# Kernel tuning notes

Measured on AMD Instinct MI355X. Metric: run time of the kernel, lower is better.

## Reference

```python
import jax, jax.numpy as jnp
import numpy as np
from jax import lax

ORDER = 2  # diffusion order per support, as in __init__(order=2)


def setup_inputs() -> dict:
    key = jax.random.key(0)
    k1, k2, k3 = jax.random.split(key, 3)
    N, C, V, L = 64, 32, 512, 13
    S, Kt, C_out = 3, 3, 32
    C_cat = (ORDER * S + 1) * C  # 224
    x = jax.random.normal(k1, (N, C, V, L), dtype=jnp.float32)
    support = jax.random.uniform(k2, (S, V, V), dtype=jnp.float32)
    # Conv2d(c_in=224, c_out=32, kernel=(1,Kt)) weights, PyTorch OIHW layout
    W = jax.random.normal(k3, (C_out, C_cat, 1, Kt), dtype=jnp.float32) * 0.02
    b = jnp.zeros((C_out,), dtype=jnp.float32)
    return {"x": x, "support": support, "W": W, "b": b}


def _nconv(x, A):
    # torch: A = A.T; einsum('ncvl,vw->ncwl', x, A.T)
    # => out[n,c,w,l] = sum_v A[w,v] * x[n,c,v,l]
    return jnp.einsum('ncvl,wv->ncwl', x, A)


def reference(x, support, W, b):
    out = [x]
    for s in range(support.shape[0]):  # small fixed support_len=3
        A = support[s]
        x1 = _nconv(x, A)
        out.append(x1)
        for _ in range(2, ORDER + 1):
            x1 = _nconv(x1, A)
            out.append(x1)
    h = jnp.concatenate(out, axis=1)  # [N, (order*S+1)*C, V, L]
    # Conv2d kernel (1, Kt), no padding, stride 1 -> temporal conv
    y = lax.conv_general_dilated(
        h, W, window_strides=(1, 1), padding='VALID',
        dimension_numbers=('NCHW', 'OIHW', 'NCHW'))
    y = y + b[None, :, None, None]
    # dropout is identity in eval mode
    return y
```

## Files before the change

kernel.cpp:

```cpp
#include <hip/hip_runtime.h>

typedef __attribute__((ext_vector_type(4))) float f32x4;
typedef __attribute__((ext_vector_type(8))) __bf16 bf16x8;
typedef __attribute__((ext_vector_type(4))) __bf16 bf16x4;
typedef __attribute__((ext_vector_type(4))) int i32x4;

#define SXE (26624 * 512)
#define AMS 262144

__global__ __launch_bounds__(256)
void prep_x(const float* __restrict__ x, __bf16* __restrict__ Xv2,
            const float* __restrict__ A, __bf16* __restrict__ Ab) {
  const int vt = blockIdx.x, n = blockIdx.y, tid = threadIdx.x;
  if (vt < 12) {
    const int i = (n * 12 + vt) * 256 + tid;
    const float4 f = ((const float4*)A)[i];
    bf16x4 o;
    o[0] = (__bf16)f.x; o[1] = (__bf16)f.y; o[2] = (__bf16)f.z; o[3] = (__bf16)f.w;
    ((bf16x4*)Ab)[i] = o;
  }
  __shared__ float Xs[32 * 209];
  const float* src = x + ((size_t)n * 32) * 6656 + vt * 16 * 13;
  for (int i = tid; i < 32 * 208; i += 256) {
    const int c = i / 208, r = i - c * 208;
    Xs[c * 209 + r] = src[(size_t)c * 6656 + r];
  }
  __syncthreads();
  for (int j = tid; j < 416; j += 256) {
    const int c = j & 31, l = j >> 5;
    bf16x8 o8[2];
    #pragma unroll
    for (int v = 0; v < 16; ++v) o8[v >> 3][v & 7] = (__bf16)Xs[c * 209 + v * 13 + l];
    __bf16* d = Xv2 + (((size_t)n * 13 + l) * 32 + c) * 512 + vt * 16;
    *(bf16x8*)d = o8[0];
    *(bf16x8*)(d + 8) = o8[1];
  }
}

__global__ __launch_bounds__(256)
void transA(const float* __restrict__ A, __bf16* __restrict__ Abt) {
  const int ut = blockIdx.x, vt = blockIdx.y, s = blockIdx.z, tid = threadIdx.x;
  __shared__ float T[64][65];
  const float* Asrc = A + (size_t)s * AMS;
  #pragma unroll
  for (int p = 0; p < 16; ++p) {
    const int rv = p * 4 + (tid >> 6), cu = tid & 63;
    T[rv][cu] = Asrc[(size_t)(vt * 64 + rv) * 512 + ut * 64 + cu];
  }
  __syncthreads();
  #pragma unroll
  for (int p = 0; p < 16; ++p) {
    const int ru = p * 4 + (tid >> 6), cv = tid & 63;
    Abt[(size_t)s * AMS + (size_t)(ut * 64 + ru) * 512 + vt * 64 + cv] = (__bf16)T[cv][ru];
  }
}

__global__ __launch_bounds__(512, 2)
void gemm_asq(const __bf16* __restrict__ Abt, const __bf16* __restrict__ Ab,
              __bf16* __restrict__ Ab2) {
  extern __shared__ char gsm[];
  const int tid = threadIdx.x;
  const int lane = tid & 63, wid = tid >> 6, q = lane >> 4, r16 = lane & 15;
  const int bx = blockIdx.x, by = blockIdx.y, s = blockIdx.z;

  const __bf16* Amat = Abt + (size_t)s * AMS;
  const __bf16* B = Ab + (size_t)s * AMS;
  __bf16* D = Ab2 + (size_t)s * AMS;

  const int W0 = by * 256, B0 = bx * 256;
  const int wm = wid >> 2, wn = wid & 3;
  const int srow = lane >> 3, spos = lane & 7;

  f32x4 acc[8][4];
  #pragma unroll
  for (int m = 0; m < 8; ++m)
    #pragma unroll
    for (int n = 0; n < 4; ++n) acc[m][n] = {0.f, 0.f, 0.f, 0.f};

  auto STAGE = [&](int bufsel, int kt) {
    const int k0 = kt * 64;
    char* As = gsm + bufsel * 65536;
    char* Bs = As + 32768;
    #pragma unroll
    for (int i = 0; i < 4; ++i) {
      const int slot = i * 8 + wid;
      const int r = slot * 8 + srow;
      const int gc = spos ^ (r & 7);
      const __bf16* ga = Amat + (size_t)(W0 + r) * 512 + k0 + gc * 8;
      const __bf16* gb = B    + (size_t)(B0 + r) * 512 + k0 + gc * 8;
      __builtin_amdgcn_global_load_lds((const __attribute__((address_space(1))) unsigned int*)ga,
                                       (__attribute__((address_space(3))) unsigned int*)(As + slot * 1024 + lane * 16),
                                       16, 0, 0);
      __builtin_amdgcn_global_load_lds((const __attribute__((address_space(1))) unsigned int*)gb,
                                       (__attribute__((address_space(3))) unsigned int*)(Bs + slot * 1024 + lane * 16),
                                       16, 0, 0);
    }
  };

  STAGE(0, 0);
  __syncthreads();
  for (int t = 0; t < 8; ++t) {
    const int cur = t & 1;
    if (t < 7) STAGE(cur ^ 1, t + 1);
    const char* As = gsm + cur * 65536;
    const char* Bs = As + 32768;
    #pragma unroll
    for (int ks = 0; ks < 2; ++ks) {
      const int ch = ks * 4 + q;
      bf16x8 af[4], df[8];
      #pragma unroll
      for (int n = 0; n < 4; ++n) {
        const int r = wn * 64 + n * 16 + r16;
        af[n] = *(const bf16x8*)(As + r * 128 + ((ch ^ (r & 7)) << 4));
      }
      #pragma unroll
      for (int m = 0; m < 8; ++m) {
        const int r = wm * 128 + m * 16 + r16;
        df[m] = *(const bf16x8*)(Bs + r * 128 + ((ch ^ (r & 7)) << 4));
      }
      #pragma unroll
      for (int m = 0; m < 8; ++m)
        #pragma unroll
        for (int n = 0; n < 4; ++n)
          acc[m][n] = __builtin_amdgcn_mfma_f32_16x16x32_bf16(af[n], df[m], acc[m][n], 0, 0, 0);
    }
    __syncthreads();
  }
  #pragma unroll
  for (int m = 0; m < 8; ++m) {
    const int b = B0 + wm * 128 + m * 16 + r16;
    #pragma unroll
    for (int n = 0; n < 4; ++n) {
      const int w = W0 + wn * 64 + n * 16 + q * 4;
      bf16x4 o4;
      o4[0] = (__bf16)acc[m][n][0]; o4[1] = (__bf16)acc[m][n][1];
      o4[2] = (__bf16)acc[m][n][2]; o4[3] = (__bf16)acc[m][n][3];
      *(bf16x4*)(D + (size_t)b * 512 + w) = o4;
    }
  }
}

__global__ __launch_bounds__(512, 2)
void gemm_bf16(const __bf16* __restrict__ Ab, const __bf16* __restrict__ Ab2,
               const __bf16* __restrict__ SRC, __bf16* __restrict__ Yb, int cpx) {
  extern __shared__ char gsm[];
  const int tid = threadIdx.x;
  const int lane = tid & 63, wid = tid >> 6, q = lane >> 4, r16 = lane & 15;

  const int bid = blockIdx.x;
  const int lg = (bid & 7) * cpx + (bid >> 3);
  const int bx = lg / 12, r12 = lg % 12, z = r12 >> 1, by = r12 & 1;

  const __bf16* Amat = (z < 3) ? (Ab + (size_t)z * AMS) : (Ab2 + (size_t)(z - 3) * AMS);
  const __bf16* B = SRC;
  __bf16* D = Yb + (size_t)z * SXE;

  const int W0 = by * 256, B0 = bx * 256;
  const int wm = wid >> 2, wn = wid & 3;
  const int srow = lane >> 3, spos = lane & 7;

  f32x4 acc[8][4];
  #pragma unroll
  for (int m = 0; m < 8; ++m)
    #pragma unroll
    for (int n = 0; n < 4; ++n) acc[m][n] = {0.f, 0.f, 0.f, 0.f};

  auto STAGE = [&](int bufsel, int kt) {
    const int k0 = kt * 64;
    char* As = gsm + bufsel * 65536;
    char* Bs = As + 32768;
    #pragma unroll
    for (int i = 0; i < 4; ++i) {
      const int slot = i * 8 + wid;
      const int r = slot * 8 + srow;
      const int gc = spos ^ (r & 7);
      const __bf16* ga = Amat + (size_t)(W0 + r) * 512 + k0 + gc * 8;
      const __bf16* gb = B    + (size_t)(B0 + r) * 512 + k0 + gc * 8;
      __builtin_amdgcn_global_load_lds((const __attribute__((address_space(1))) unsigned int*)ga,
                                       (__attribute__((address_space(3))) unsigned int*)(As + slot * 1024 + lane * 16),
                                       16, 0, 0);
      __builtin_amdgcn_global_load_lds((const __attribute__((address_space(1))) unsigned int*)gb,
                                       (__attribute__((address_space(3))) unsigned int*)(Bs + slot * 1024 + lane * 16),
                                       16, 0, 0);
    }
  };

  STAGE(0, 0);
  __syncthreads();

  for (int t = 0; t < 8; ++t) {
    const int cur = t & 1;
    if (t < 7) STAGE(cur ^ 1, t + 1);
    const char* As = gsm + cur * 65536;
    const char* Bs = As + 32768;
    #pragma unroll
    for (int ks = 0; ks < 2; ++ks) {
      const int ch = ks * 4 + q;
      bf16x8 af[4], df[8];
      #pragma unroll
      for (int n = 0; n < 4; ++n) {
        const int r = wn * 64 + n * 16 + r16;
        af[n] = *(const bf16x8*)(As + r * 128 + ((ch ^ (r & 7)) << 4));
      }
      #pragma unroll
      for (int m = 0; m < 8; ++m) {
        const int r = wm * 128 + m * 16 + r16;
        df[m] = *(const bf16x8*)(Bs + r * 128 + ((ch ^ (r & 7)) << 4));
      }
      __builtin_amdgcn_s_setprio(1);
      #pragma unroll
      for (int m = 0; m < 8; ++m)
        #pragma unroll
        for (int n = 0; n < 4; ++n)
          acc[m][n] = __builtin_amdgcn_mfma_f32_16x16x32_bf16(af[n], df[m], acc[m][n], 0, 0, 0);
      __builtin_amdgcn_s_setprio(0);
    }
    __syncthreads();
  }

  #pragma unroll
  for (int m = 0; m < 8; ++m) {
    const int b = B0 + wm * 128 + m * 16 + r16;
    #pragma unroll
    for (int n = 0; n < 4; ++n) {
      const int w = W0 + wn * 64 + n * 16 + q * 4;
      bf16x4 o4;
      o4[0] = (__bf16)acc[m][n][0]; o4[1] = (__bf16)acc[m][n][1];
      o4[2] = (__bf16)acc[m][n][2]; o4[3] = (__bf16)acc[m][n][3];
      *(bf16x4*)(D + (size_t)b * 512 + w) = o4;
    }
  }
}

__global__ __launch_bounds__(256, 2)
void conv_kernel(const __bf16* __restrict__ Xv2, const __bf16* __restrict__ Y1,
                 const __bf16* __restrict__ Y2, const float* __restrict__ W,
                 const float* __restrict__ bias, float* __restrict__ y) {
  const int vt = blockIdx.x;
  const int n  = blockIdx.y;
  const int tid = threadIdx.x;
  const int lane = tid & 63, wave = tid >> 6, q = lane >> 4, r16 = lane & 15;

  __shared__ char sm[59392];
  char* Ws = sm + 53248;

  const __bf16* gsrc[7] = {Xv2, Y1, Y2, Y1 + (size_t)SXE, Y2 + (size_t)SXE,
                           Y1 + 2 * (size_t)SXE, Y2 + 2 * (size_t)SXE};

  f32x4 acc[11][2];
  #pragma unroll
  for (int t = 0; t < 11; ++t) { acc[t][0] = {0,0,0,0}; acc[t][1] = {0,0,0,0}; }

  const int vv = wave * 16 + r16;
  const int vch = vv >> 3;
  const int vlo = (vv & 7) * 2;
  const int cst = tid >> 3, hst = tid & 7;
  const size_t goff = ((size_t)cst << 9) + hst * 8;
  const int lds_off = cst * 128 + ((hst ^ ((cst >> 3) << 1)) << 4);
  const int gbase = q * 1024 + (((vch ^ (q << 1)) & 7) << 4) + vlo;

  const size_t base = ((size_t)n * 416) * 512 + vt * 64;

  i32x4 hreg[13];
  {
    const __bf16* src = gsrc[0] + base;
    #pragma unroll
    for (int l = 0; l < 13; ++l)
      hreg[l] = *(const i32x4*)(src + (size_t)l * 16384 + goff);
  }

  for (int g = 0; g < 7; ++g) {
    __syncthreads();
    #pragma unroll
    for (int l = 0; l < 13; ++l)
      *(i32x4*)(sm + l * 4096 + lds_off) = hreg[l];
    for (int idx = tid; idx < 768; idx += 256) {
      const int f = idx >> 7, rem2 = idx & 127, lw = rem2 >> 1, half = rem2 & 1;
      const int kt = f >> 1, of = f & 1;
      const int o = of * 16 + (lw & 15);
      const int cc = g * 32 + (lw >> 4) * 8 + half * 4;
      bf16x4 w4;
      #pragma unroll
      for (int j = 0; j < 4; ++j)
        w4[j] = (__bf16)W[((size_t)o * 224 + cc + j) * 3 + kt];
      *(bf16x4*)(Ws + idx * 8) = w4;
    }
    __syncthreads();

    if (g < 6) {
      const __bf16* srcn = gsrc[g + 1] + base;
      #pragma unroll
      for (int l = 0; l < 13; ++l)
        hreg[l] = *(const i32x4*)(srcn + (size_t)l * 16384 + goff);
    }

    bf16x8 a8[13];
    #pragma unroll
    for (int l = 0; l < 13; ++l) {
      bf16x8 a;
      #pragma unroll
      for (int j = 0; j < 8; ++j)
        a[j] = *(const __bf16*)(sm + l * 4096 + gbase + j * 128);
      a8[l] = a;
    }
    bf16x8 wf[6];
    #pragma unroll
    for (int f = 0; f < 6; ++f)
      wf[f] = *(const bf16x8*)(Ws + (f * 64 + lane) * 16);

    #pragma unroll
    for (int kt = 0; kt < 3; ++kt)
      #pragma unroll
      for (int of = 0; of < 2; ++of)
        #pragma unroll
        for (int t = 0; t < 11; ++t)
          acc[t][of] = __builtin_amdgcn_mfma_f32_16x16x32_bf16(a8[t + kt], wf[kt * 2 + of], acc[t][of], 0, 0, 0);
  }

  float* Ds = (float*)sm;
  const int o16 = lane & 15;
  #pragma unroll
  for (int p = 0; p < 2; ++p) {
    __syncthreads();
    #pragma unroll
    for (int t = 0; t < 11; ++t) {
      const int vbase = wave * 16 + q * 4;
      #pragma unroll
      for (int rg = 0; rg < 4; ++rg)
        Ds[o16 * 708 + (vbase + rg) * 11 + t] = acc[t][p][rg];
    }
    __syncthreads();
    #pragma unroll
    for (int i = 0; i < 11; ++i) {
      const int cg = tid + i * 256;
      const int oo = cg / 176, ch = cg - oo * 176;
      f32x4 v4 = *(const f32x4*)(Ds + oo * 708 + ch * 4);
      const float bo = bias[p * 16 + oo];
      v4[0] += bo; v4[1] += bo; v4[2] += bo; v4[3] += bo;
      float* yp = y + (((size_t)n * 32 + p * 16 + oo) * 512 + vt * 64) * 11 + ch * 4;
      *(f32x4*)yp = v4;
    }
  }
}

extern "C" void kernel_launch(void* const* d_in, const int* in_sizes, int n_in,
                              void* d_out, int out_size, void* d_ws, size_t ws_size,
                              hipStream_t stream) {
  (void)in_sizes; (void)n_in; (void)out_size; (void)ws_size;
  const float* x = (const float*)d_in[0];
  const float* A = (const float*)d_in[1];
  const float* W = (const float*)d_in[2];
  const float* b = (const float*)d_in[3];
  float* y = (float*)d_out;

  char* ws = (char*)d_ws;
  const size_t SXB = (size_t)SXE * 2;
  __bf16* Xv2 = (__bf16*)ws;
  __bf16* Y1  = (__bf16*)(ws + SXB);
  __bf16* Y2  = (__bf16*)(ws + 4 * SXB);
  __bf16* Ab  = (__bf16*)(ws + 7 * SXB);
  __bf16* Ab2 = (__bf16*)d_out;
  __bf16* Abt = (__bf16*)((char*)d_out + (4 << 20));

  prep_x<<<dim3(32, 64), 256, 0, stream>>>(x, Xv2, A, Ab);
  transA<<<dim3(8, 8, 3), 256, 0, stream>>>(A, Abt);
  gemm_asq<<<dim3(2, 2, 3), 512, 131072, stream>>>(Abt, Ab, Ab2);
  gemm_bf16<<<dim3(1248), 512, 131072, stream>>>(Ab, Ab2, Xv2, Y1, 156);
  conv_kernel<<<dim3(8, 64), 256, 0, stream>>>(Xv2, Y1, Y2, W, b, y);
}
```

Baseline: 208.8 us.

## Apply temporal conv before graph diffusion and fuse diffusion GEMMs with accumulation

This reorders the computation using linearity. The channel/temporal convolution is applied first to X for each of the 7 hop groups, giving smaller projected tensors P with 32 channels and 11 time steps. A single GEMM then sums A_z·P_z over the 6 diffusion operators along a concatenated K dimension, and adds the identity term and bias in its epilogue. This drops the large Y intermediates and their re-read by the conv, and it lowers total MFMA work. The cost is a smaller 128x128 GEMM tile with a long 48-step K loop, plus epilogue stores strided by 11 floats that may coalesce poorly.

```diff
diff --git a/kernel.cpp b/kernel.cpp
--- a/kernel.cpp
+++ b/kernel.cpp
@@ -5,8 +5,8 @@
 typedef __attribute__((ext_vector_type(4))) __bf16 bf16x4;
 typedef __attribute__((ext_vector_type(4))) int i32x4;
 
-#define SXE (26624 * 512)
 #define AMS 262144
+#define PSZ (22528 * 512)
 
 __global__ __launch_bounds__(256)
 void prep_x(const float* __restrict__ x, __bf16* __restrict__ Xv2,
@@ -140,102 +140,9 @@
   }
 }
 
-__global__ __launch_bounds__(512, 2)
-void gemm_bf16(const __bf16* __restrict__ Ab, const __bf16* __restrict__ Ab2,
-               const __bf16* __restrict__ SRC, __bf16* __restrict__ Yb, int cpx) {
-  extern __shared__ char gsm[];
-  const int tid = threadIdx.x;
-  const int lane = tid & 63, wid = tid >> 6, q = lane >> 4, r16 = lane & 15;
-
-  const int bid = blockIdx.x;
-  const int lg = (bid & 7) * cpx + (bid >> 3);
-  const int bx = lg / 12, r12 = lg % 12, z = r12 >> 1, by = r12 & 1;
-
-  const __bf16* Amat = (z < 3) ? (Ab + (size_t)z * AMS) : (Ab2 + (size_t)(z - 3) * AMS);
-  const __bf16* B = SRC;
-  __bf16* D = Yb + (size_t)z * SXE;
-
-  const int W0 = by * 256, B0 = bx * 256;
-  const int wm = wid >> 2, wn = wid & 3;
-  const int srow = lane >> 3, spos = lane & 7;
-
-  f32x4 acc[8][4];
-  #pragma unroll
-  for (int m = 0; m < 8; ++m)
-    #pragma unroll
-    for (int n = 0; n < 4; ++n) acc[m][n] = {0.f, 0.f, 0.f, 0.f};
-
-  auto STAGE = [&](int bufsel, int kt) {
-    const int k0 = kt * 64;
-    char* As = gsm + bufsel * 65536;
-    char* Bs = As + 32768;
-    #pragma unroll
-    for (int i = 0; i < 4; ++i) {
-      const int slot = i * 8 + wid;
-      const int r = slot * 8 + srow;
-      const int gc = spos ^ (r & 7);
-      const __bf16* ga = Amat + (size_t)(W0 + r) * 512 + k0 + gc * 8;
-      const __bf16* gb = B    + (size_t)(B0 + r) * 512 + k0 + gc * 8;
-      __builtin_amdgcn_global_load_lds((const __attribute__((address_space(1))) unsigned int*)ga,
-                                       (__attribute__((address_space(3))) unsigned int*)(As + slot * 1024 + lane * 16),
-                                       16, 0, 0);
-      __builtin_amdgcn_global_load_lds((const __attribute__((address_space(1))) unsigned int*)gb,
-                                       (__attribute__((address_space(3))) unsigned int*)(Bs + slot * 1024 + lane * 16),
-                                       16, 0, 0);
-    }
-  };
-
-  STAGE(0, 0);
-  __syncthreads();
-
-  for (int t = 0; t < 8; ++t) {
-    const int cur = t & 1;
-    if (t < 7) STAGE(cur ^ 1, t + 1);
-    const char* As = gsm + cur * 65536;
-    const char* Bs = As + 32768;
-    #pragma unroll
-    for (int ks = 0; ks < 2; ++ks) {
-      const int ch = ks * 4 + q;
-      bf16x8 af[4], df[8];
-      #pragma unroll
-      for (int n = 0; n < 4; ++n) {
-        const int r = wn * 64 + n * 16 + r16;
-        af[n] = *(const bf16x8*)(As + r * 128 + ((ch ^ (r & 7)) << 4));
-      }
-      #pragma unroll
-      for (int m = 0; m < 8; ++m) {
-        const int r = wm * 128 + m * 16 + r16;
-        df[m] = *(const bf16x8*)(Bs + r * 128 + ((ch ^ (r & 7)) << 4));
-      }
-      __builtin_amdgcn_s_setprio(1);
-      #pragma unroll
-      for (int m = 0; m < 8; ++m)
-        #pragma unroll
-        for (int n = 0; n < 4; ++n)
-          acc[m][n] = __builtin_amdgcn_mfma_f32_16x16x32_bf16(af[n], df[m], acc[m][n], 0, 0, 0);
-      __builtin_amdgcn_s_setprio(0);
-    }
-    __syncthreads();
-  }
-
-  #pragma unroll
-  for (int m = 0; m < 8; ++m) {
-    const int b = B0 + wm * 128 + m * 16 + r16;
-    #pragma unroll
-    for (int n = 0; n < 4; ++n) {
-      const int w = W0 + wn * 64 + n * 16 + q * 4;
-      bf16x4 o4;
-      o4[0] = (__bf16)acc[m][n][0]; o4[1] = (__bf16)acc[m][n][1];
-      o4[2] = (__bf16)acc[m][n][2]; o4[3] = (__bf16)acc[m][n][3];
-      *(bf16x4*)(D + (size_t)b * 512 + w) = o4;
-    }
-  }
-}
-
 __global__ __launch_bounds__(256, 2)
-void conv_kernel(const __bf16* __restrict__ Xv2, const __bf16* __restrict__ Y1,
-                 const __bf16* __restrict__ Y2, const float* __restrict__ W,
-                 const float* __restrict__ bias, float* __restrict__ y) {
+void pconv(const __bf16* __restrict__ Xv2, const float* __restrict__ W,
+           __bf16* __restrict__ P) {
   const int vt = blockIdx.x;
   const int n  = blockIdx.y;
   const int tid = threadIdx.x;
@@ -243,13 +150,6 @@
 
   __shared__ char sm[59392];
   char* Ws = sm + 53248;
-
-  const __bf16* gsrc[7] = {Xv2, Y1, Y2, Y1 + (size_t)SXE, Y2 + (size_t)SXE,
-                           Y1 + 2 * (size_t)SXE, Y2 + 2 * (size_t)SXE};
-
-  f32x4 acc[11][2];
-  #pragma unroll
-  for (int t = 0; t < 11; ++t) { acc[t][0] = {0,0,0,0}; acc[t][1] = {0,0,0,0}; }
 
   const int vv = wave * 16 + r16;
   const int vch = vv >> 3;
@@ -259,21 +159,26 @@
   const int lds_off = cst * 128 + ((hst ^ ((cst >> 3) << 1)) << 4);
   const int gbase = q * 1024 + (((vch ^ (q << 1)) & 7) << 4) + vlo;
 
-  const size_t base = ((size_t)n * 416) * 512 + vt * 64;
-
-  i32x4 hreg[13];
-  {
-    const __bf16* src = gsrc[0] + base;
-    #pragma unroll
-    for (int l = 0; l < 13; ++l)
-      hreg[l] = *(const i32x4*)(src + (size_t)l * 16384 + goff);
+  const __bf16* src = Xv2 + ((size_t)n * 416) * 512 + vt * 64;
+  #pragma unroll
+  for (int l = 0; l < 13; ++l) {
+    i32x4 val = *(const i32x4*)(src + (size_t)l * 16384 + goff);
+    *(i32x4*)(sm + l * 4096 + lds_off) = val;
+  }
+  __syncthreads();
+
+  bf16x8 a8[13];
+  #pragma unroll
+  for (int l = 0; l < 13; ++l) {
+    bf16x8 a;
+    #pragma unroll
+    for (int j = 0; j < 8; ++j)
+      a[j] = *(const __bf16*)(sm + l * 4096 + gbase + j * 128);
+    a8[l] = a;
   }
 
   for (int g = 0; g < 7; ++g) {
     __syncthreads();
-    #pragma unroll
-    for (int l = 0; l < 13; ++l)
-      *(i32x4*)(sm + l * 4096 + lds_off) = hreg[l];
     for (int idx = tid; idx < 768; idx += 256) {
       const int f = idx >> 7, rem2 = idx & 127, lw = rem2 >> 1, half = rem2 & 1;
       const int kt = f >> 1, of = f & 1;
@@ -287,27 +192,14 @@
     }
     __syncthreads();
 
-    if (g < 6) {
-      const __bf16* srcn = gsrc[g + 1] + base;
-      #pragma unroll
-      for (int l = 0; l < 13; ++l)
-        hreg[l] = *(const i32x4*)(srcn + (size_t)l * 16384 + goff);
-    }
-
-    bf16x8 a8[13];
-    #pragma unroll
-    for (int l = 0; l < 13; ++l) {
-      bf16x8 a;
-      #pragma unroll
-      for (int j = 0; j < 8; ++j)
-        a[j] = *(const __bf16*)(sm + l * 4096 + gbase + j * 128);
-      a8[l] = a;
-    }
     bf16x8 wf[6];
     #pragma unroll
     for (int f = 0; f < 6; ++f)
       wf[f] = *(const bf16x8*)(Ws + (f * 64 + lane) * 16);
 
+    f32x4 acc[11][2];
+    #pragma unroll
+    for (int t = 0; t < 11; ++t) { acc[t][0] = {0,0,0,0}; acc[t][1] = {0,0,0,0}; }
     #pragma unroll
     for (int kt = 0; kt < 3; ++kt)
       #pragma unroll
@@ -315,30 +207,114 @@
         #pragma unroll
         for (int t = 0; t < 11; ++t)
           acc[t][of] = __builtin_amdgcn_mfma_f32_16x16x32_bf16(a8[t + kt], wf[kt * 2 + of], acc[t][of], 0, 0, 0);
-  }
-
-  float* Ds = (float*)sm;
-  const int o16 = lane & 15;
-  #pragma unroll
-  for (int p = 0; p < 2; ++p) {
+
+    __bf16* Pg = P + (size_t)g * PSZ;
+    #pragma unroll
+    for (int of = 0; of < 2; ++of) {
+      const int o = of * 16 + r16;
+      #pragma unroll
+      for (int t = 0; t < 11; ++t) {
+        bf16x4 o4;
+        o4[0] = (__bf16)acc[t][of][0]; o4[1] = (__bf16)acc[t][of][1];
+        o4[2] = (__bf16)acc[t][of][2]; o4[3] = (__bf16)acc[t][of][3];
+        *(bf16x4*)(Pg + ((((size_t)n * 32 + o) * 11 + t) << 9) + vt * 64 + wave * 16 + q * 4) = o4;
+      }
+    }
+  }
+}
+
+__global__ __launch_bounds__(256, 2)
+void gemm_acc(const __bf16* __restrict__ Ab, const __bf16* __restrict__ Ab2,
+              const __bf16* __restrict__ P, const float* __restrict__ bias,
+              float* __restrict__ y, int cpx) {
+  extern __shared__ char gsm[];
+  const int tid = threadIdx.x;
+  const int lane = tid & 63, wave = tid >> 6, q = lane >> 4, r16 = lane & 15;
+
+  const int bid = blockIdx.x;
+  const int lg = (bid & 7) * cpx + (bid >> 3);
+  const int bx = lg >> 2, by = lg & 3;
+
+  const int W0 = by * 128, B0 = bx * 128;
+  const int wm = wave >> 1, wn = wave & 1;
+  const int srow = lane >> 3, spos = lane & 7;
+
+  f32x4 acc[4][4];
+  #pragma unroll
+  for (int m = 0; m < 4; ++m)
+    #pragma unroll
+    for (int n = 0; n < 4; ++n) acc[m][n] = {0.f, 0.f, 0.f, 0.f};
+
+  auto STAGE = [&](int bufsel, int step) {
+    const int z = step >> 3, kt = step & 7;
+    const int k0 = kt * 64;
+    const __bf16* Az = ((z & 1) ? Ab2 : Ab) + (size_t)(z >> 1) * AMS;
+    const __bf16* Pz = P + (size_t)(z + 1) * PSZ;
+    char* As = gsm + bufsel * 32768;
+    char* Bs = As + 16384;
+    #pragma unroll
+    for (int i = 0; i < 4; ++i) {
+      const int slot = i * 4 + wave;
+      const int r = slot * 8 + srow;
+      const int gc = spos ^ (r & 7);
+      const __bf16* ga = Az + (size_t)(W0 + r) * 512 + k0 + gc * 8;
+      const __bf16* gb = Pz + (size_t)(B0 + r) * 512 + k0 + gc * 8;
+      __builtin_amdgcn_global_load_lds((const __attribute__((address_space(1))) unsigned int*)ga,
+                                       (__attribute__((address_space(3))) unsigned int*)(As + slot * 1024 + lane * 16),
+                                       16, 0, 0);
+      __builtin_amdgcn_global_load_lds((const __attribute__((address_space(1))) unsigned int*)gb,
+                                       (__attribute__((address_space(3))) unsigned int*)(Bs + slot * 1024 + lane * 16),
+                                       16, 0, 0);
+    }
+  };
+
+  STAGE(0, 0);
+  __syncthreads();
+
+  for (int t = 0; t < 48; ++t) {
+    const int cur = t & 1;
+    if (t < 47) STAGE(cur ^ 1, t + 1);
+    const char* As = gsm + cur * 32768;
+    const char* Bs = As + 16384;
+    #pragma unroll
+    for (int ks = 0; ks < 2; ++ks) {
+      const int ch = ks * 4 + q;
+      bf16x8 af[4], df[4];
+      #pragma unroll
+      for (int m = 0; m < 4; ++m) {
+        const int r = wm * 64 + m * 16 + r16;
+        af[m] = *(const bf16x8*)(As + r * 128 + ((ch ^ (r & 7)) << 4));
+      }
+      #pragma unroll
+      for (int n = 0; n < 4; ++n) {
+        const int r = wn * 64 + n * 16 + r16;
+        df[n] = *(const bf16x8*)(Bs + r * 128 + ((ch ^ (r & 7)) << 4));
+      }
+      __builtin_amdgcn_s_setprio(1);
+      #pragma unroll
+      for (int m = 0; m < 4; ++m)
+        #pragma unroll
+        for (int n = 0; n < 4; ++n)
+          acc[m][n] = __builtin_amdgcn_mfma_f32_16x16x32_bf16(af[m], df[n], acc[m][n], 0, 0, 0);
+      __builtin_amdgcn_s_setprio(0);
+    }
     __syncthreads();
-    #pragma unroll
-    for (int t = 0; t < 11; ++t) {
-      const int vbase = wave * 16 + q * 4;
+  }
+
+  #pragma unroll
+  for (int m = 0; m < 4; ++m) {
+    const int w = W0 + wm * 64 + m * 16 + q * 4;
+    #pragma unroll
+    for (int n = 0; n < 4; ++n) {
+      const unsigned b = B0 + wn * 64 + n * 16 + r16;
+      const bf16x4 p0 = *(const bf16x4*)(P + (size_t)b * 512 + w);
+      const unsigned yrow = b / 11u;
+      const unsigned tt = b - yrow * 11u;
+      const float bo = bias[yrow & 31u];
+      float* yp = y + (size_t)yrow * 5632 + (size_t)w * 11 + tt;
       #pragma unroll
       for (int rg = 0; rg < 4; ++rg)
-        Ds[o16 * 708 + (vbase + rg) * 11 + t] = acc[t][p][rg];
-    }
-    __syncthreads();
-    #pragma unroll
-    for (int i = 0; i < 11; ++i) {
-      const int cg = tid + i * 256;
-      const int oo = cg / 176, ch = cg - oo * 176;
-      f32x4 v4 = *(const f32x4*)(Ds + oo * 708 + ch * 4);
-      const float bo = bias[p * 16 + oo];
-      v4[0] += bo; v4[1] += bo; v4[2] += bo; v4[3] += bo;
-      float* yp = y + (((size_t)n * 32 + p * 16 + oo) * 512 + vt * 64) * 11 + ch * 4;
-      *(f32x4*)yp = v4;
+        yp[(size_t)rg * 11] = acc[m][n][rg] + (float)p0[rg] + bo;
     }
   }
 }
@@ -354,17 +330,15 @@
   float* y = (float*)d_out;
 
   char* ws = (char*)d_ws;
-  const size_t SXB = (size_t)SXE * 2;
   __bf16* Xv2 = (__bf16*)ws;
-  __bf16* Y1  = (__bf16*)(ws + SXB);
-  __bf16* Y2  = (__bf16*)(ws + 4 * SXB);
-  __bf16* Ab  = (__bf16*)(ws + 7 * SXB);
-  __bf16* Ab2 = (__bf16*)d_out;
-  __bf16* Abt = (__bf16*)((char*)d_out + (4 << 20));
+  __bf16* P   = (__bf16*)(ws + 27262976);
+  __bf16* Ab  = (__bf16*)(ws + 27262976 + 161480704);
+  __bf16* Ab2 = (__bf16*)(ws + 27262976 + 161480704 + 1572864);
+  __bf16* Abt = (__bf16*)d_out;
 
   prep_x<<<dim3(32, 64), 256, 0, stream>>>(x, Xv2, A, Ab);
   transA<<<dim3(8, 8, 3), 256, 0, stream>>>(A, Abt);
   gemm_asq<<<dim3(2, 2, 3), 512, 131072, stream>>>(Abt, Ab, Ab2);
-  gemm_bf16<<<dim3(1248), 512, 131072, stream>>>(Ab, Ab2, Xv2, Y1, 156);
-  conv_kernel<<<dim3(8, 64), 256, 0, stream>>>(Xv2, Y1, Y2, W, b, y);
-}
+  pconv<<<dim3(8, 64), 256, 0, stream>>>(Xv2, W, P);
+  gemm_acc<<<dim3(704), 256, 65536, stream>>>(Ab, Ab2, P, b, y, 88);
+}
```

New measurement: 274.9 us. 31.6% more time.
